# Kernel optimization log

Measured on AMD Instinct MI355X. Metric: run time of the kernel, lower is better.

## Reference

```python
import jax, jax.numpy as jnp
import numpy as np
from jax import lax

T = 3650      # days
H = 256       # MLP hidden width
N_IN = 4      # [s_snow, s_water, prcp, tmean]
N_OUT = 5     # [p_snow, p_rain, m, et, q]
DT = 1.0      # euler step (days), equals forcing sampling interval


def setup_inputs() -> dict:
    key = jax.random.key(0)
    ks = jax.random.split(key, 8)
    # inputs[:, 0]=s_snow init traj, [:,1]=s_water, [:,2]=prcp, [:,3]=tmean, [:,4]=time
    data = jax.random.normal(ks[0], (T, 4), dtype=jnp.float32)
    data = data.at[:, 2].set(jnp.abs(data[:, 2]))  # prcp >= 0
    time = jnp.arange(T, dtype=jnp.float32)[:, None]
    inputs = jnp.concatenate([data, time], axis=-1)  # [T, 5]
    dayl = jax.random.uniform(ks[1], (T,), dtype=jnp.float32)  # day length fraction
    s = 0.1  # small init keeps sinh/exp transforms stable over the long rollout
    W0 = jax.random.normal(ks[2], (N_IN, H), dtype=jnp.float32) * (s / np.sqrt(N_IN))
    b0 = jnp.zeros((H,), dtype=jnp.float32)
    W1 = jax.random.normal(ks[3], (H, H), dtype=jnp.float32) * (s / np.sqrt(H))
    b1 = jnp.zeros((H,), dtype=jnp.float32)
    W2 = jax.random.normal(ks[4], (H, H), dtype=jnp.float32) * (s / np.sqrt(H))
    b2 = jnp.zeros((H,), dtype=jnp.float32)
    Wout = jax.random.normal(ks[5], (H, N_OUT), dtype=jnp.float32) * (s / np.sqrt(H))
    bout = jnp.zeros((N_OUT,), dtype=jnp.float32)
    return {"inputs": inputs, "dayl": dayl, "W0": W0, "b0": b0, "W1": W1,
            "b1": b1, "W2": W2, "b2": b2, "Wout": Wout, "bout": bout}


def _step_function(x):
    return (jnp.tanh(5.0 * x) + 1.0) * 0.5


def reference(inputs, dayl, W0, b0, W1, b1, W2, b2, Wout, bout):
    prcp = inputs[:, 2]
    tmean = inputs[:, 3]
    s_snow0 = inputs[0, 0]
    s_water0 = inputs[0, 1]

    def mlp(x):  # x: [..., N_IN] -> [..., N_OUT]
        h = jnp.tanh(x @ W0 + b0)
        h = jnp.tanh(h @ W1 + b1)
        h = jnpp_tanh(h @ W2 + b2) if False else jnp.tanh(h @ W2 + b2)
        return h @ Wout + bout

    def derivs(s0, s1, p, tm, ld):
        o = mlp(jnp.stack([s0, s1, p, tm]))  # [5]
        p_snow, p_rain, m, et, q = o[0], o[1], o[2], o[3], o[4]
        # scale_target_vars transform path
        p_snow = jax.nn.relu(jnp.sinh(p_snow) * _step_function(-tm))
        p_rain = jax.nn.relu(jnp.sinh(p_rain))
        m = jax.nn.relu(_step_function(s0) * jnp.sinh(m))
        et = _step_function(s1) * jnp.exp(et) * ld
        q = _step_function(s1) * jnp.exp(q)
        return p_snow - m, p_rain + m - et - q

    def body(carry, xs):
        s0, s1 = carry
        p, tm, ld = xs
        d0, d1 = derivs(s0, s1, p, tm, ld)
        ns0 = s0 + DT * d0
        ns1 = s1 + DT * d1
        return (ns0, ns1), (ns0, ns1)

    xs = (prcp[:-1], tmean[:-1], dayl[:-1])
    _, (ss, sw) = lax.scan(body, (s_snow0, s_water0), xs)
    s_snow_nn = jnp.concatenate([s_snow0[None], ss])    # [T]
    s_water_nn = jnp.concatenate([s_water0[None], sw])  # [T]

    inputs_nn = jnp.stack([s_snow_nn, s_water_nn, prcp, tmean], axis=-1)  # [T, 4]
    q_output = mlp(inputs_nn)[:, -1]  # last head = q
    return (q_output, s_snow_nn, s_water_nn)
```

## Files before the change

### kernel.cpp

```cpp
#include <hip/hip_runtime.h>
#include <hip/hip_bf16.h>

#define TT 3650
#define HH 256

typedef _Float16 f16x4 __attribute__((ext_vector_type(4)));
typedef _Float16 f16x8 __attribute__((ext_vector_type(8)));
typedef float f32x4 __attribute__((ext_vector_type(4)));

__device__ __forceinline__ float xexp2(float x) { return __builtin_amdgcn_exp2f(x); }
__device__ __forceinline__ float xrcp(float x) { return __builtin_amdgcn_rcpf(x); }
__device__ __forceinline__ float xexp(float x) { return xexp2(x * 1.4426950408889634f); }
__device__ __forceinline__ float xtanh(float x) {
  float e = xexp2(x * 2.8853900817779268f);
  return 1.0f - 2.0f * xrcp(e + 1.0f);
}
__device__ __forceinline__ float xstep(float x) {
  return xrcp(1.0f + xexp2(-14.426950408889634f * x));
}
__device__ __forceinline__ float xsinh(float x) {
  float e = xexp(x);
  return 0.5f * (e - xrcp(e));
}

#define DPPADD(x, ctrl)                                                        \
  (x) += __builtin_bit_cast(float, __builtin_amdgcn_update_dpp(                \
            0, __builtin_bit_cast(int, (x)), (ctrl), 0xf, 0xf, false));
#define RDLANE(x, l)                                                           \
  __builtin_bit_cast(float,                                                    \
      __builtin_amdgcn_readlane(__builtin_bit_cast(int, (x)), (l)))

#define REP8(M) M(0) M(1) M(2) M(3) M(4) M(5) M(6) M(7)
#define REPC(M) M(0) M(1) M(2) M(3)

#define WSCALE 1024.0f
#define WDESCALE 0.0009765625f

#define SF_PAD 2

__global__ void __launch_bounds__(256, 1) exphydro_scan(
    const float* __restrict__ gin, const float* __restrict__ gdayl,
    const float* __restrict__ gW0, const float* __restrict__ gb0,
    const float* __restrict__ gW1, const float* __restrict__ gb1,
    const float* __restrict__ gW2, const float* __restrict__ gb2,
    const float* __restrict__ gWout, const float* __restrict__ gbout,
    float* __restrict__ gout) {
  __shared__ alignas(16) _Float16 h0l[HH];
  __shared__ alignas(16) _Float16 h1l[HH];
  __shared__ float sWP[64];
  __shared__ f32x4 sF[TT + SF_PAD];
  __shared__ float sQ[TT], sS0[TT], sS1[TT];

  const int tid = threadIdx.x;
  const int lane = tid & 63;
  const int w = tid >> 6;
  const int li = lane & 15;
  const int g = lane >> 4;
  const int jb = 64 * w + 4 * li;

  for (int i = tid; i < TT; i += 256) {
    f32x4 F = {gin[5 * i + 2], gin[5 * i + 3], gdayl[i], 0.0f};
    sF[i] = F;
  }
  if (tid < 2 * SF_PAD) {
    f32x4 Z = {0.f, 0.f, 0.f, 0.f};
    sF[TT + tid - ((tid < SF_PAD) ? 0 : SF_PAD)] = Z;
  }
  if (tid < 64) sWP[tid] = 0.0f;

  float s0 = gin[0], s1 = gin[1];
  const float bo0 = gbout[0], bo1 = gbout[1], bo2 = gbout[2], bo3 = gbout[3],
              bo4 = gbout[4];
#define CDECL(c)                                                               \
  const float w00_##c = gW0[jb + (c)], w01_##c = gW0[HH + jb + (c)],           \
              w02_##c = gW0[2 * HH + jb + (c)],                                \
              w03_##c = gW0[3 * HH + jb + (c)], b0_##c = gb0[jb + (c)],        \
              b1_##c = gb1[jb + (c)], b2_##c = gb2[jb + (c)],                  \
              wo0_##c = gWout[5 * (jb + (c)) + 0],                             \
              wo1_##c = gWout[5 * (jb + (c)) + 1],                             \
              wo2_##c = gWout[5 * (jb + (c)) + 2],                             \
              wo3_##c = gWout[5 * (jb + (c)) + 3],                             \
              wo4_##c = gWout[5 * (jb + (c)) + 4];
  REPC(CDECL)
#undef CDECL

#define FDECL(i) f16x8 a1_0_##i, a1_1_##i, a1_2_##i, a1_3_##i,                 \
                       a2_0_##i, a2_1_##i, a2_2_##i, a2_3_##i;
  REP8(FDECL)
#undef FDECL
#define MK(dst, G, i, c)                                                       \
  {                                                                            \
    const float* p = (G) + (32 * (i) + g * 8) * HH + jb + (c);                 \
    f16x8 f;                                                                   \
    f[0] = (_Float16)(p[0] * WSCALE);      f[1] = (_Float16)(p[HH] * WSCALE);  \
    f[2] = (_Float16)(p[2 * HH] * WSCALE); f[3] = (_Float16)(p[3 * HH] * WSCALE); \
    f[4] = (_Float16)(p[4 * HH] * WSCALE); f[5] = (_Float16)(p[5 * HH] * WSCALE); \
    f[6] = (_Float16)(p[6 * HH] * WSCALE); f[7] = (_Float16)(p[7 * HH] * WSCALE); \
    dst = f;                                                                   \
    asm volatile("" : "+a"(dst));                                              \
  }
#define FINIT(i)                                                               \
  MK(a1_0_##i, gW1, i, 0) MK(a1_1_##i, gW1, i, 1)                              \
  MK(a1_2_##i, gW1, i, 2) MK(a1_3_##i, gW1, i, 3)                              \
  MK(a2_0_##i, gW2, i, 0) MK(a2_1_##i, gW2, i, 1)                              \
  MK(a2_2_##i, gW2, i, 2) MK(a2_3_##i, gW2, i, 3)
  REP8(FINIT)
#undef FINIT
#undef MK

  const char* hp0 = (const char*)h0l + g * 16;
  const char* hp1 = (const char*)h1l + g * 16;

#define MFMA(acc, a, b)                                                        \
  asm("v_mfma_f32_16x16x32_f16 %0, %1, %2, %0" : "+v"(acc) : "v"(a), "a"(b));

  __syncthreads();

  f32x4 Fc = sF[0];
  for (int t = 0; t < TT; ++t) {
    const float p_in = Fc[0];
    const float tm = Fc[1];
    const float ld = Fc[2];

#define L0C(c)                                                                 \
  float h0_##c =                                                               \
      xtanh(b0_##c + s0 * w00_##c + s1 * w01_##c + p_in * w02_##c + tm * w03_##c);
    REPC(L0C)
#undef L0C
    if (lane < 16) {
      f16x4 hv = {(_Float16)h0_0, (_Float16)h0_1, (_Float16)h0_2,
                  (_Float16)h0_3};
      *(f16x4*)((char*)h0l + (jb << 1)) = hv;
    }
    __syncthreads();

    f32x4 Fn = sF[t + 1];

    f32x4 d0 = {0.f, 0.f, 0.f, 0.f}, d1 = {0.f, 0.f, 0.f, 0.f};
    f32x4 d2 = {0.f, 0.f, 0.f, 0.f}, d3 = {0.f, 0.f, 0.f, 0.f};
    asm volatile("s_nop 1" : "+v"(d0), "+v"(d1), "+v"(d2), "+v"(d3));
#define MM1(i)                                                                 \
  {                                                                            \
    f16x8 av = *(const f16x8*)(hp0 + (i) * 64);                                \
    MFMA(d0, av, a1_0_##i) MFMA(d1, av, a1_1_##i)                              \
    MFMA(d2, av, a1_2_##i) MFMA(d3, av, a1_3_##i)                              \
  }
    REP8(MM1)
#undef MM1
    asm volatile("s_nop 7\n\ts_nop 7" : "+v"(d0), "+v"(d1), "+v"(d2), "+v"(d3));
#define H1C(c) float h1_##c = xtanh(d##c[0] * WDESCALE + b1_##c);
    REPC(H1C)
#undef H1C
    if (lane < 16) {
      f16x4 hv = {(_Float16)h1_0, (_Float16)h1_1, (_Float16)h1_2,
                  (_Float16)h1_3};
      *(f16x4*)((char*)h1l + (jb << 1)) = hv;
    }
    __syncthreads();

    f32x4 e0 = {0.f, 0.f, 0.f, 0.f}, e1 = {0.f, 0.f, 0.f, 0.f};
    f32x4 e2 = {0.f, 0.f, 0.f, 0.f}, e3 = {0.f, 0.f, 0.f, 0.f};
    asm volatile("s_nop 1" : "+v"(e0), "+v"(e1), "+v"(e2), "+v"(e3));
#define MM2(i)                                                                 \
  {                                                                            \
    f16x8 av = *(const f16x8*)(hp1 + (i) * 64);                                \
    MFMA(e0, av, a2_0_##i) MFMA(e1, av, a2_1_##i)                              \
    MFMA(e2, av, a2_2_##i) MFMA(e3, av, a2_3_##i)                              \
  }
    REP8(MM2)
#undef MM2
    asm volatile("s_nop 7\n\ts_nop 7" : "+v"(e0), "+v"(e1), "+v"(e2), "+v"(e3));
#define H2C(c) float h2_##c = xtanh(e##c[0] * WDESCALE + b2_##c);
    REPC(H2C)
#undef H2C

    float p0 = h2_0 * wo0_0 + h2_1 * wo0_1 + h2_2 * wo0_2 + h2_3 * wo0_3;
    float p1 = h2_0 * wo1_0 + h2_1 * wo1_1 + h2_2 * wo1_2 + h2_3 * wo1_3;
    float p2 = h2_0 * wo2_0 + h2_1 * wo2_1 + h2_2 * wo2_2 + h2_3 * wo2_3;
    float p3 = h2_0 * wo3_0 + h2_1 * wo3_1 + h2_2 * wo3_2 + h2_3 * wo3_3;
    float p4 = h2_0 * wo4_0 + h2_1 * wo4_1 + h2_2 * wo4_2 + h2_3 * wo4_3;
    DPPADD(p0, 0x121) DPPADD(p0, 0x122) DPPADD(p0, 0x124) DPPADD(p0, 0x128)
    DPPADD(p1, 0x121) DPPADD(p1, 0x122) DPPADD(p1, 0x124) DPPADD(p1, 0x128)
    DPPADD(p2, 0x121) DPPADD(p2, 0x122) DPPADD(p2, 0x124) DPPADD(p2, 0x128)
    DPPADD(p3, 0x121) DPPADD(p3, 0x122) DPPADD(p3, 0x124) DPPADD(p3, 0x128)
    DPPADD(p4, 0x121) DPPADD(p4, 0x122) DPPADD(p4, 0x124) DPPADD(p4, 0x128)
    float pv = lane == 0 ? p0 : lane == 1 ? p1 : lane == 2 ? p2
                                          : lane == 3 ? p3 : p4;
    if (lane < 5) sWP[lane * 4 + w] = pv;
    __syncthreads();

    float v = sWP[lane];
    DPPADD(v, 0xB1)
    DPPADD(v, 0x4E)
    float o0 = RDLANE(v, 0) + bo0;
    float o1 = RDLANE(v, 4) + bo1;
    float o2 = RDLANE(v, 8) + bo2;
    float o3 = RDLANE(v, 12) + bo3;
    float o4 = RDLANE(v, 16) + bo4;
    if (tid == 64) {
      sQ[t] = o4;
      sS0[t] = s0;
      sS1[t] = s1;
    }
    float sh0 = xsinh(o0), sh1 = xsinh(o1), sh2 = xsinh(o2);
    float e3x = xexp(o3), e4x = xexp(o4);
    float stn = xstep(-tm), st0 = xstep(s0), st1 = xstep(s1);
    float psn = fmaxf(sh0 * stn, 0.0f);
    float prn = fmaxf(sh1, 0.0f);
    float mm = fmaxf(st0 * sh2, 0.0f);
    float evt = st1 * e3x * ld;
    float qq = st1 * e4x;
    s0 += psn - mm;
    s1 += prn + mm - evt - qq;
    Fc = Fn;
  }
#undef MFMA

  __syncthreads();
  for (int i = tid; i < TT; i += 256) {
    gout[i] = sQ[i];
    gout[TT + i] = sS0[i];
    gout[2 * TT + i] = sS1[i];
  }
}

extern "C" void kernel_launch(void* const* d_in, const int* in_sizes, int n_in,
                              void* d_out, int out_size, void* d_ws, size_t ws_size,
                              hipStream_t stream) {
  const float* gin   = (const float*)d_in[0];
  const float* gdayl = (const float*)d_in[1];
  const float* gW0   = (const float*)d_in[2];
  const float* gb0   = (const float*)d_in[3];
  const float* gW1   = (const float*)d_in[4];
  const float* gb1   = (const float*)d_in[5];
  const float* gW2   = (const float*)d_in[6];
  const float* gb2   = (const float*)d_in[7];
  const float* gWout = (const float*)d_in[8];
  const float* gbout = (const float*)d_in[9];
  float* gout = (float*)d_out;
  exphydro_scan<<<dim3(1), dim3(256), 0, stream>>>(
      gin, gdayl, gW0, gb0, gW1, gb1, gW2, gb2, gWout, gbout, gout);
}
```

Measured before the change: 4.829 ms.

## Split hidden columns across eight waves to shorten per-wave MFMA chains

Launches 512 threads instead of 256, so each wave owns 2 hidden columns per layer instead of 4. This halves the serial MFMA chain and the tanh work each wave does per timestep. The cross-wave output reduction is rewritten to use a row rotate, a swizzle and readlanes over 8 waves. The cost is more waves taking part in each of the three block barriers per step on this latency-bound sequential scan.

```diff
diff --git a/kernel.cpp b/kernel.cpp
--- a/kernel.cpp
+++ b/kernel.cpp
@@ -4,7 +4,6 @@
 #define TT 3650
 #define HH 256
 
-typedef _Float16 f16x4 __attribute__((ext_vector_type(4)));
 typedef _Float16 f16x8 __attribute__((ext_vector_type(8)));
 typedef float f32x4 __attribute__((ext_vector_type(4)));
 
@@ -31,14 +30,13 @@
       __builtin_amdgcn_readlane(__builtin_bit_cast(int, (x)), (l)))
 
 #define REP8(M) M(0) M(1) M(2) M(3) M(4) M(5) M(6) M(7)
-#define REPC(M) M(0) M(1) M(2) M(3)
 
 #define WSCALE 1024.0f
 #define WDESCALE 0.0009765625f
 
 #define SF_PAD 2
 
-__global__ void __launch_bounds__(256, 1) exphydro_scan(
+__global__ void __launch_bounds__(512) exphydro_scan(
     const float* __restrict__ gin, const float* __restrict__ gdayl,
     const float* __restrict__ gW0, const float* __restrict__ gb0,
     const float* __restrict__ gW1, const float* __restrict__ gb1,
@@ -56,36 +54,35 @@
   const int w = tid >> 6;
   const int li = lane & 15;
   const int g = lane >> 4;
-  const int jb = 64 * w + 4 * li;
-
-  for (int i = tid; i < TT; i += 256) {
+  const int jb = 32 * w + 2 * li;
+
+  for (int i = tid; i < TT; i += 512) {
     f32x4 F = {gin[5 * i + 2], gin[5 * i + 3], gdayl[i], 0.0f};
     sF[i] = F;
   }
-  if (tid < 2 * SF_PAD) {
+  if (tid < SF_PAD) {
     f32x4 Z = {0.f, 0.f, 0.f, 0.f};
-    sF[TT + tid - ((tid < SF_PAD) ? 0 : SF_PAD)] = Z;
+    sF[TT + tid] = Z;
   }
   if (tid < 64) sWP[tid] = 0.0f;
 
   float s0 = gin[0], s1 = gin[1];
   const float bo0 = gbout[0], bo1 = gbout[1], bo2 = gbout[2], bo3 = gbout[3],
               bo4 = gbout[4];
-#define CDECL(c)                                                               \
-  const float w00_##c = gW0[jb + (c)], w01_##c = gW0[HH + jb + (c)],           \
-              w02_##c = gW0[2 * HH + jb + (c)],                                \
-              w03_##c = gW0[3 * HH + jb + (c)], b0_##c = gb0[jb + (c)],        \
-              b1_##c = gb1[jb + (c)], b2_##c = gb2[jb + (c)],                  \
-              wo0_##c = gWout[5 * (jb + (c)) + 0],                             \
-              wo1_##c = gWout[5 * (jb + (c)) + 1],                             \
-              wo2_##c = gWout[5 * (jb + (c)) + 2],                             \
-              wo3_##c = gWout[5 * (jb + (c)) + 3],                             \
-              wo4_##c = gWout[5 * (jb + (c)) + 4];
-  REPC(CDECL)
-#undef CDECL
-
-#define FDECL(i) f16x8 a1_0_##i, a1_1_##i, a1_2_##i, a1_3_##i,                 \
-                       a2_0_##i, a2_1_##i, a2_2_##i, a2_3_##i;
+  const float w00_0 = gW0[jb], w01_0 = gW0[HH + jb], w02_0 = gW0[2 * HH + jb],
+              w03_0 = gW0[3 * HH + jb];
+  const float w00_1 = gW0[jb + 1], w01_1 = gW0[HH + jb + 1],
+              w02_1 = gW0[2 * HH + jb + 1], w03_1 = gW0[3 * HH + jb + 1];
+  const float b0_0 = gb0[jb], b1_0 = gb1[jb], b2_0 = gb2[jb];
+  const float b0_1 = gb0[jb + 1], b1_1 = gb1[jb + 1], b2_1 = gb2[jb + 1];
+  const float wo0_0 = gWout[5 * jb + 0], wo1_0 = gWout[5 * jb + 1],
+              wo2_0 = gWout[5 * jb + 2], wo3_0 = gWout[5 * jb + 3],
+              wo4_0 = gWout[5 * jb + 4];
+  const float wo0_1 = gWout[5 * jb + 5], wo1_1 = gWout[5 * jb + 6],
+              wo2_1 = gWout[5 * jb + 7], wo3_1 = gWout[5 * jb + 8],
+              wo4_1 = gWout[5 * jb + 9];
+
+#define FDECL(i) f16x8 a1_0_##i, a1_1_##i, a2_0_##i, a2_1_##i;
   REP8(FDECL)
 #undef FDECL
 #define MK(dst, G, i, c)                                                       \
@@ -101,9 +98,7 @@
   }
 #define FINIT(i)                                                               \
   MK(a1_0_##i, gW1, i, 0) MK(a1_1_##i, gW1, i, 1)                              \
-  MK(a1_2_##i, gW1, i, 2) MK(a1_3_##i, gW1, i, 3)                              \
-  MK(a2_0_##i, gW2, i, 0) MK(a2_1_##i, gW2, i, 1)                              \
-  MK(a2_2_##i, gW2, i, 2) MK(a2_3_##i, gW2, i, 3)
+  MK(a2_0_##i, gW2, i, 0) MK(a2_1_##i, gW2, i, 1)
   REP8(FINIT)
 #undef FINIT
 #undef MK
@@ -122,63 +117,58 @@
     const float tm = Fc[1];
     const float ld = Fc[2];
 
-#define L0C(c)                                                                 \
-  float h0_##c =                                                               \
-      xtanh(b0_##c + s0 * w00_##c + s1 * w01_##c + p_in * w02_##c + tm * w03_##c);
-    REPC(L0C)
-#undef L0C
+    float h0_0 =
+        xtanh(b0_0 + s0 * w00_0 + s1 * w01_0 + p_in * w02_0 + tm * w03_0);
+    float h0_1 =
+        xtanh(b0_1 + s0 * w00_1 + s1 * w01_1 + p_in * w02_1 + tm * w03_1);
     if (lane < 16) {
-      f16x4 hv = {(_Float16)h0_0, (_Float16)h0_1, (_Float16)h0_2,
-                  (_Float16)h0_3};
-      *(f16x4*)((char*)h0l + (jb << 1)) = hv;
+      unsigned hw =
+          (unsigned)__builtin_bit_cast(unsigned short, (_Float16)h0_0) |
+          ((unsigned)__builtin_bit_cast(unsigned short, (_Float16)h0_1) << 16);
+      *(unsigned*)((char*)h0l + (jb << 1)) = hw;
     }
     __syncthreads();
 
     f32x4 Fn = sF[t + 1];
 
     f32x4 d0 = {0.f, 0.f, 0.f, 0.f}, d1 = {0.f, 0.f, 0.f, 0.f};
-    f32x4 d2 = {0.f, 0.f, 0.f, 0.f}, d3 = {0.f, 0.f, 0.f, 0.f};
-    asm volatile("s_nop 1" : "+v"(d0), "+v"(d1), "+v"(d2), "+v"(d3));
+    asm volatile("s_nop 1" : "+v"(d0), "+v"(d1));
 #define MM1(i)                                                                 \
   {                                                                            \
     f16x8 av = *(const f16x8*)(hp0 + (i) * 64);                                \
     MFMA(d0, av, a1_0_##i) MFMA(d1, av, a1_1_##i)                              \
-    MFMA(d2, av, a1_2_##i) MFMA(d3, av, a1_3_##i)                              \
   }
     REP8(MM1)
 #undef MM1
-    asm volatile("s_nop 7\n\ts_nop 7" : "+v"(d0), "+v"(d1), "+v"(d2), "+v"(d3));
-#define H1C(c) float h1_##c = xtanh(d##c[0] * WDESCALE + b1_##c);
-    REPC(H1C)
-#undef H1C
+    asm volatile("s_nop 7\n\ts_nop 7" : "+v"(d0), "+v"(d1));
+    float h1_0 = xtanh(d0[0] * WDESCALE + b1_0);
+    float h1_1 = xtanh(d1[0] * WDESCALE + b1_1);
     if (lane < 16) {
-      f16x4 hv = {(_Float16)h1_0, (_Float16)h1_1, (_Float16)h1_2,
-                  (_Float16)h1_3};
-      *(f16x4*)((char*)h1l + (jb << 1)) = hv;
+      unsigned hw =
+          (unsigned)__builtin_bit_cast(unsigned short, (_Float16)h1_0) |
+          ((unsigned)__builtin_bit_cast(unsigned short, (_Float16)h1_1) << 16);
+      *(unsigned*)((char*)h1l + (jb << 1)) = hw;
     }
     __syncthreads();
 
     f32x4 e0 = {0.f, 0.f, 0.f, 0.f}, e1 = {0.f, 0.f, 0.f, 0.f};
-    f32x4 e2 = {0.f, 0.f, 0.f, 0.f}, e3 = {0.f, 0.f, 0.f, 0.f};
-    asm volatile("s_nop 1" : "+v"(e0), "+v"(e1), "+v"(e2), "+v"(e3));
+    asm volatile("s_nop 1" : "+v"(e0), "+v"(e1));
 #define MM2(i)                                                                 \
   {                                                                            \
     f16x8 av = *(const f16x8*)(hp1 + (i) * 64);                                \
     MFMA(e0, av, a2_0_##i) MFMA(e1, av, a2_1_##i)                              \
-    MFMA(e2, av, a2_2_##i) MFMA(e3, av, a2_3_##i)                              \
   }
     REP8(MM2)
 #undef MM2
-    asm volatile("s_nop 7\n\ts_nop 7" : "+v"(e0), "+v"(e1), "+v"(e2), "+v"(e3));
-#define H2C(c) float h2_##c = xtanh(e##c[0] * WDESCALE + b2_##c);
-    REPC(H2C)
-#undef H2C
-
-    float p0 = h2_0 * wo0_0 + h2_1 * wo0_1 + h2_2 * wo0_2 + h2_3 * wo0_3;
-    float p1 = h2_0 * wo1_0 + h2_1 * wo1_1 + h2_2 * wo1_2 + h2_3 * wo1_3;
-    float p2 = h2_0 * wo2_0 + h2_1 * wo2_1 + h2_2 * wo2_2 + h2_3 * wo2_3;
-    float p3 = h2_0 * wo3_0 + h2_1 * wo3_1 + h2_2 * wo3_2 + h2_3 * wo3_3;
-    float p4 = h2_0 * wo4_0 + h2_1 * wo4_1 + h2_2 * wo4_2 + h2_3 * wo4_3;
+    asm volatile("s_nop 7\n\ts_nop 7" : "+v"(e0), "+v"(e1));
+    float h2_0 = xtanh(e0[0] * WDESCALE + b2_0);
+    float h2_1 = xtanh(e1[0] * WDESCALE + b2_1);
+
+    float p0 = h2_0 * wo0_0 + h2_1 * wo0_1;
+    float p1 = h2_0 * wo1_0 + h2_1 * wo1_1;
+    float p2 = h2_0 * wo2_0 + h2_1 * wo2_1;
+    float p3 = h2_0 * wo3_0 + h2_1 * wo3_1;
+    float p4 = h2_0 * wo4_0 + h2_1 * wo4_1;
     DPPADD(p0, 0x121) DPPADD(p0, 0x122) DPPADD(p0, 0x124) DPPADD(p0, 0x128)
     DPPADD(p1, 0x121) DPPADD(p1, 0x122) DPPADD(p1, 0x124) DPPADD(p1, 0x128)
     DPPADD(p2, 0x121) DPPADD(p2, 0x122) DPPADD(p2, 0x124) DPPADD(p2, 0x128)
@@ -186,17 +176,18 @@
     DPPADD(p4, 0x121) DPPADD(p4, 0x122) DPPADD(p4, 0x124) DPPADD(p4, 0x128)
     float pv = lane == 0 ? p0 : lane == 1 ? p1 : lane == 2 ? p2
                                           : lane == 3 ? p3 : p4;
-    if (lane < 5) sWP[lane * 4 + w] = pv;
+    if (lane < 5) sWP[w * 8 + lane] = pv;
     __syncthreads();
 
     float v = sWP[lane];
-    DPPADD(v, 0xB1)
-    DPPADD(v, 0x4E)
-    float o0 = RDLANE(v, 0) + bo0;
-    float o1 = RDLANE(v, 4) + bo1;
-    float o2 = RDLANE(v, 8) + bo2;
-    float o3 = RDLANE(v, 12) + bo3;
-    float o4 = RDLANE(v, 16) + bo4;
+    DPPADD(v, 0x128)
+    v += __builtin_bit_cast(
+        float, __builtin_amdgcn_ds_swizzle(__builtin_bit_cast(int, v), 0x401F));
+    float o0 = RDLANE(v, 0) + RDLANE(v, 32) + bo0;
+    float o1 = RDLANE(v, 1) + RDLANE(v, 33) + bo1;
+    float o2 = RDLANE(v, 2) + RDLANE(v, 34) + bo2;
+    float o3 = RDLANE(v, 3) + RDLANE(v, 35) + bo3;
+    float o4 = RDLANE(v, 4) + RDLANE(v, 36) + bo4;
     if (tid == 64) {
       sQ[t] = o4;
       sS0[t] = s0;
@@ -217,7 +208,7 @@
 #undef MFMA
 
   __syncthreads();
-  for (int i = tid; i < TT; i += 256) {
+  for (int i = tid; i < TT; i += 512) {
     gout[i] = sQ[i];
     gout[TT + i] = sS0[i];
     gout[2 * TT + i] = sS1[i];
@@ -238,6 +229,6 @@
   const float* gWout = (const float*)d_in[8];
   const float* gbout = (const float*)d_in[9];
   float* gout = (float*)d_out;
-  exphydro_scan<<<dim3(1), dim3(256), 0, stream>>>(
+  exphydro_scan<<<dim3(1), dim3(512), 0, stream>>>(
       gin, gdayl, gW0, gb0, gW1, gb1, gW2, gb2, gWout, gbout, gout);
 }
```

Measured after the change: 5.277 ms. 9.3% more time.
